# Performance work log

Hardware: AMD Instinct MI355X
Metric: run time of the kernel (lower is better)

The kernel has to match this reference:

```python
import jax, jax.numpy as jnp
import numpy as np

B, D, L, T, K = 16, 256, 256, 1000, 3
DW, DC = 4, 2  # dim_w, dim_c
CH = 8         # ConvSwishBlock out channels (10 = 1 start + 1 end + 8)


def swish(x):
    return x * jax.nn.sigmoid(x)


def setup_inputs() -> dict:
    key = jax.random.key(0)
    ks = jax.random.split(key, 12)
    # durations ~ U[1,6] per phone -> sum ~ 3.5*L ~ 896 <= T
    durations = 1.0 + 5.0 * jax.random.uniform(ks[0], (B, L), dtype=jnp.float32)
    phoneme = jax.random.normal(ks[1], (B, D, L), dtype=jnp.float32)
    # True = padded phone position
    phone_len = L - (jnp.arange(B) % 4) * 16
    phoneme_mask = (jnp.arange(L)[None, :] >= phone_len[:, None])[:, None, :]
    durations = jnp.where(phoneme_mask[:, 0, :], 0.0, durations)
    s = 0.02
    p = {
        'proj_w_W': s * jax.random.normal(ks[2], (D, D)), 'proj_w_b': jnp.zeros((D,)),
        'conv_w_W': s * jax.random.normal(ks[3], (CH, D, K)), 'conv_w_b': jnp.zeros((CH,)),
        'mlp_w_W': s * jax.random.normal(ks[4], (2 + CH, DW)), 'mlp_w_b': jnp.zeros((DW,)),
        'lin_w_W': s * jax.random.normal(ks[5], (D * DW, D)), 'lin_w_b': jnp.zeros((D,)),
        'proj_c_W': s * jax.random.normal(ks[6], (D, D)), 'proj_c_b': jnp.zeros((D,)),
        'conv_c_W': s * jax.random.normal(ks[7], (CH, D, K)), 'conv_c_b': jnp.zeros((CH,)),
        'mlp_c_W': s * jax.random.normal(ks[8], (2 + CH, DC)), 'mlp_c_b': jnp.zeros((DC,)),
        'lin_c_W': s * jax.random.normal(ks[9], (DW * DC, D)), 'lin_c_b': jnp.zeros((D,)),
    }
    return {'durations': durations, 'phoneme': phoneme, 'phoneme_mask': phoneme_mask, **p}


def _conv_branch(x, phone_pad, projW, projb, convW, convb):
    # x: (B, D, L). 1x1 conv projection, then K-wide 'same' conv to CH channels, swish, mask.
    x = jnp.einsum('od,bdl->bol', projW, x) + projb[None, :, None]
    h = jax.lax.conv_general_dilated(x, convW, (1,), 'SAME',
                                     dimension_numbers=('NCH', 'OIH', 'NCH'))
    h = swish(h + convb[None, :, None])
    h = jnp.where(phone_pad[:, None, :], 0.0, h)
    return h.transpose(0, 2, 1)  # (B, L, CH)


def _forward(durations, phoneme, phoneme_mask,
             proj_w_W, proj_w_b, conv_w_W, conv_w_b, mlp_w_W, mlp_w_b, lin_w_W, lin_w_b,
             proj_c_W, proj_c_b, conv_c_W, conv_c_b, mlp_c_W, mlp_c_b, lin_c_W, lin_c_b):
    phone_pad = phoneme_mask[:, 0, :]                       # (B, L) True = pad
    frame_len = jnp.clip(jnp.round(jnp.sum(durations, -1)), 0, T).astype(jnp.int32)
    frame_pad = jnp.arange(T)[None, :] >= frame_len[:, None]  # (B, T) True = pad
    attn_pad = frame_pad[:, :, None] | phone_pad[:, None, :]  # (B, T, L)

    sd = jnp.cumsum(durations, -1)                          # (B, L) cumulative end times
    sk = sd - durations                                     # (B, L) start times
    t = jnp.arange(1, T + 1, dtype=durations.dtype)
    S = jnp.where(attn_pad, 0.0, t[None, :, None] - sk[:, None, :])                    # (B,T,L)
    E = jnp.where(attn_pad, 0.0, jnp.broadcast_to(sd[:, None, :], attn_pad.shape)
                  - sk[:, None, :])                                                    # (B,T,L)

    # W branch: per-(frame, phone) attention weights over phones
    h_w = _conv_branch(phoneme, phone_pad, proj_w_W, proj_w_b, conv_w_W, conv_w_b)     # (B,L,CH)
    feat_w = jnp.concatenate(
        [S[..., None], E[..., None], jnp.broadcast_to(h_w[:, None], (B, T, L, CH))], -1)
    w = swish(feat_w @ mlp_w_W + mlp_w_b)                   # (B, T, L, DW)
    w = jnp.where(phone_pad[:, None, :, None], -jnp.inf, w)
    w = jax.nn.softmax(w, axis=2)                           # softmax over phones
    w = jnp.where(frame_pad[:, :, None, None], 0.0, w)

    # C branch: auxiliary per-(frame, phone) context
    h_c = _conv_branch(phoneme, phone_pad, proj_c_W, proj_c_b, conv_c_W, conv_c_b)
    feat_c = jnp.concatenate(
        [S[..., None], E[..., None], jnp.broadcast_to(h_c[:, None], (B, T, L, CH))], -1)
    c = swish(feat_c @ mlp_c_W + mlp_c_b)                   # (B, T, L, DC)

    # combine: wh = einsum over phones with phoneme features, wc with c matrix
    wh = jnp.einsum('btnq,bnh->btqh', w, phoneme.transpose(0, 2, 1))  # (B,T,DW,D)
    wh = wh.reshape(B, T, DW * D) @ lin_w_W + lin_w_b                 # (B,T,D)
    wc = jnp.einsum('btnq,btnp->btqp', w, c)                          # (B,T,DW,DC)
    wc = wc.reshape(B, T, DW * DC) @ lin_c_W + lin_c_b                # (B,T,D)
    return wh + wc


def reference(durations, phoneme, phoneme_mask,
              proj_w_W, proj_w_b, conv_w_W, conv_w_b, mlp_w_W, mlp_w_b, lin_w_W, lin_w_b,
              proj_c_W, proj_c_b, conv_c_W, conv_c_b, mlp_c_W, mlp_c_b, lin_c_W, lin_c_b):
    return _forward(durations, phoneme, phoneme_mask,
                    proj_w_W, proj_w_b, conv_w_W, conv_w_b, mlp_w_W, mlp_w_b, lin_w_W, lin_w_b,
                    proj_c_W, proj_c_b, conv_c_W, conv_c_b, mlp_c_W, mlp_c_b, lin_c_W, lin_c_b)
```

## Files before the change

kernel.cpp:

```cpp
#include <hip/hip_runtime.h>


typedef short v8s __attribute__((ext_vector_type(8)));
typedef _Float16 v8h __attribute__((ext_vector_type(8)));
typedef float f4 __attribute__((ext_vector_type(4)));

__device__ __forceinline__ float bf2f(unsigned short h) {
  return __uint_as_float(((unsigned int)h) << 16);
}
__device__ __forceinline__ unsigned short f2bf(float f) {
  unsigned int u = __float_as_uint(f);
  u = (u + 0x7FFFu + ((u >> 16) & 1u)) >> 16;
  return (unsigned short)u;
}
__device__ __forceinline__ float swishf(float x) {
  return x * __builtin_amdgcn_rcpf(1.f + __expf(-x));
}

__global__ __launch_bounds__(256) void k_prep(
    const float* __restrict__ dur, const float* __restrict__ ph,
    const float* __restrict__ liWw,
    const float* __restrict__ cvWw, const float* __restrict__ pjWw,
    const float* __restrict__ pjbw,
    const float* __restrict__ cvWc, const float* __restrict__ pjWc,
    const float* __restrict__ pjbc,
    float* __restrict__ sk, int* __restrict__ frame_len,
    unsigned short* __restrict__ Mb, float* __restrict__ bK,
    unsigned short* __restrict__ LWT, unsigned short* __restrict__ phT) {
  __shared__ float sm[32 * 33];
  int blk = blockIdx.x, tid = threadIdx.x;
  if (blk < 16) {
    int b = blk, l = tid;
    float d = dur[b * 256 + l];
    sm[l] = d;
    __syncthreads();
    for (int off = 1; off < 256; off <<= 1) {
      float v = (l >= off) ? sm[l - off] : 0.f;
      __syncthreads();
      sm[l] += v;
      __syncthreads();
    }
    sk[b * 256 + l] = sm[l] - d;
    if (l == 255) {
      int fl = (int)rintf(sm[255]);
      frame_len[b] = min(max(fl, 0), 1000);
    }
  } else if (blk < 64) {
    int x = blk - 16;
    int br = x / 24, ck = x % 24;
    int ch = ck / 3, k = ck % 3;
    const float* convW = br ? cvWc : cvWw;
    const float* projW = br ? pjWc : pjWw;
    const float* projb = br ? pjbc : pjbw;
    int d = tid;
    float acc = 0.f;
    for (int o = 0; o < 256; o++)
      acc += convW[ch * 768 + o * 3 + k] * projW[o * 256 + d];
    Mb[(br * 24 + ck) * 256 + d] = f2bf(acc);
    if (d == 0) {
      float bb = 0.f;
      for (int o = 0; o < 256; o++)
        bb += convW[ch * 768 + o * 3 + k] * projb[o];
      bK[br * 24 + ck] = bb;
    }
  } else if (blk < 320) {
    int idx = blk - 64;
    int kt = idx & 31, ot = idx >> 5;
    int tx = tid & 31, ty = tid >> 5;
#pragma unroll
    for (int r = 0; r < 4; r++) {
      int row = ty + r * 8;
      sm[row * 33 + tx] = liWw[(size_t)(kt * 32 + row) * 256 + ot * 32 + tx];
    }
    __syncthreads();
#pragma unroll
    for (int r = 0; r < 4; r++) {
      int row = ty + r * 8;
      LWT[(size_t)(ot * 32 + row) * 1024 + kt * 32 + tx] =
          f2bf(sm[tx * 33 + row]);
    }
  } else {
    int idx = blk - 320;
    int ht = idx & 7, lt = (idx >> 3) & 7, b = idx >> 6;
    int tx = tid & 31, ty = tid >> 5;
#pragma unroll
    for (int r = 0; r < 4; r++) {
      int row = ty + r * 8;
      sm[row * 33 + tx] =
          ph[(size_t)b * 65536 + (size_t)(ht * 32 + row) * 256 + lt * 32 + tx];
    }
    __syncthreads();
#pragma unroll
    for (int r = 0; r < 4; r++) {
      int row = ty + r * 8;
      phT[(size_t)b * 65536 + (size_t)(lt * 32 + row) * 256 + ht * 32 + tx] =
          f2bf(sm[tx * 33 + row]);
    }
  }
}

__global__ __launch_bounds__(256) void k_convG(
    const unsigned short* __restrict__ phT, const unsigned short* __restrict__ Mb,
    const float* __restrict__ bK, const float* __restrict__ cvbw,
    const float* __restrict__ cvbc, const float* __restrict__ dur,
    const unsigned short* __restrict__ LWT,
    float* __restrict__ hw, float* __restrict__ hc,
    _Float16* __restrict__ G) {
  __shared__ __align__(16) float C[256 * 49];
  int blk = blockIdx.x;
  int tid = threadIdx.x, wave = tid >> 6, lane = tid & 63;
  int quad = lane >> 4, col = lane & 15;
  if (blk < 16) {
    int b = blk;
    int l0 = wave * 64;
    const unsigned short* Ab = phT + (size_t)b * 65536;
    f4 acc[4][3] = {};
#pragma unroll
    for (int k0 = 0; k0 < 256; k0 += 32) {
      v8s af[4], bf[3];
#pragma unroll
      for (int lt = 0; lt < 4; lt++)
        af[lt] = *(const v8s*)(Ab + (size_t)(l0 + lt * 16 + col) * 256 + k0 + quad * 8);
#pragma unroll
      for (int ct = 0; ct < 3; ct++)
        bf[ct] = *(const v8s*)(Mb + (size_t)(ct * 16 + col) * 256 + k0 + quad * 8);
#pragma unroll
      for (int lt = 0; lt < 4; lt++)
#pragma unroll
        for (int ct = 0; ct < 3; ct++)
          acc[lt][ct] = __builtin_amdgcn_mfma_f32_16x16x32_bf16(af[lt], bf[ct],
                                                                acc[lt][ct], 0, 0, 0);
    }
#pragma unroll
    for (int lt = 0; lt < 4; lt++)
#pragma unroll
      for (int ct = 0; ct < 3; ct++)
#pragma unroll
        for (int r = 0; r < 4; r++)
          C[(l0 + lt * 16 + quad * 4 + r) * 49 + ct * 16 + col] = acc[lt][ct][r];
    __syncthreads();
    int l = tid;
    float dv = dur[b * 256 + l];
    bool vld = (dv != 0.f);
#pragma unroll
    for (int br = 0; br < 2; br++) {
      const float* convb = br ? cvbc : cvbw;
      float* dst = br ? hc : hw;
#pragma unroll
      for (int ch = 0; ch < 8; ch++) {
        int ck = br * 24 + ch * 3;
        float v = convb[ch] + bK[ck + 1] + C[l * 49 + ck + 1];
        if (l > 0) v += bK[ck + 0] + C[(l - 1) * 49 + ck + 0];
        if (l < 255) v += bK[ck + 2] + C[(l + 1) * 49 + ck + 2];
        v = swishf(v);
        dst[((size_t)(b * 256 + l)) * 8 + ch] = vld ? v : 0.f;
      }
    }
  } else {
    int idx = blk - 16;
    int b = idx >> 4;
    int sub = idx & 15;
    int q = sub >> 2, quadr = sub & 3;
    int mo = (quadr >> 1) * 128, nl = (quadr & 1) * 128;
    int wm = (wave & 1) * 64, wn = (wave >> 1) * 64;
    const unsigned short* Ag = LWT + (size_t)q * 256;
    const unsigned short* Bg = phT + (size_t)b * 65536;
    f4 acc[4][4] = {};
#pragma unroll
    for (int k0 = 0; k0 < 256; k0 += 32) {
      v8s af[4], bf[4];
#pragma unroll
      for (int mt = 0; mt < 4; mt++)
        af[mt] = *(const v8s*)(Ag + (size_t)(mo + wm + mt * 16 + col) * 1024 +
                               k0 + quad * 8);
#pragma unroll
      for (int nt = 0; nt < 4; nt++)
        bf[nt] = *(const v8s*)(Bg + (size_t)(nl + wn + nt * 16 + col) * 256 +
                               k0 + quad * 8);
#pragma unroll
      for (int mt = 0; mt < 4; mt++)
#pragma unroll
        for (int nt = 0; nt < 4; nt++)
          acc[mt][nt] = __builtin_amdgcn_mfma_f32_16x16x32_bf16(af[mt], bf[nt],
                                                                acc[mt][nt], 0, 0, 0);
    }
    _Float16* Gb = G + (size_t)b * 262144 + q * 256;
#pragma unroll
    for (int mt = 0; mt < 4; mt++)
#pragma unroll
      for (int r = 0; r < 4; r++) {
        int orow = mo + wm + mt * 16 + quad * 4 + r;
#pragma unroll
        for (int nt = 0; nt < 4; nt++) {
          int lcol = nl + wn + nt * 16 + col;
          Gb[(size_t)orow * 1024 + lcol] = (_Float16)acc[mt][nt][r];
        }
      }
  }
}

__global__ __launch_bounds__(256, 4) void k_fuse(
    const _Float16* __restrict__ G,
    const float* __restrict__ dur, const float* __restrict__ sk,
    const int* __restrict__ frame_len,
    const float* __restrict__ hw, const float* __restrict__ hc,
    const float* __restrict__ mlpWw, const float* __restrict__ mlpbw,
    const float* __restrict__ mlpWc, const float* __restrict__ mlpbc,
    const float* __restrict__ lwb, const float* __restrict__ lcb,
    const float* __restrict__ LC, float* __restrict__ out) {
  __shared__ __align__(16) _Float16 Et[2][16][264];
  __shared__ __align__(16) float4 Lbw4[256];
  __shared__ __align__(16) float4 Laux4[256];
  __shared__ float4 wredM[4];
  __shared__ float invL[16 * 4];
  __shared__ float wcL[16 * 8];

  int blk = blockIdx.x;
  int b = (blk & 7) * 2 + ((blk >> 3) & 1);
  int tile = blk >> 4;
  int t0 = tile * 16;
  int tid = threadIdx.x, wave = tid >> 6, lane = tid & 63;
  int quad = lane >> 4, col = lane & 15;

  {
    int l = tid;
    float4 a0 = *(const float4*)&hw[((size_t)(b * 256 + l)) * 8];
    float4 a1 = *(const float4*)&hw[((size_t)(b * 256 + l)) * 8 + 4];
    float4 c0 = *(const float4*)&hc[((size_t)(b * 256 + l)) * 8];
    float4 c1 = *(const float4*)&hc[((size_t)(b * 256 + l)) * 8 + 4];
    float hwv[8] = {a0.x, a0.y, a0.z, a0.w, a1.x, a1.y, a1.z, a1.w};
    float hcv[8] = {c0.x, c0.y, c0.z, c0.w, c1.x, c1.y, c1.z, c1.w};
    float dl = dur[b * 256 + l];
    float skl = sk[b * 256 + l];
    float msk = (dl != 0.f) ? 1.f : 0.f;
    float A[4];
#pragma unroll
    for (int q = 0; q < 4; q++) {
      float a = mlpbw[q] + dl * mlpWw[4 + q] - skl * mlpWw[q];
#pragma unroll
      for (int ch = 0; ch < 8; ch++) a += hwv[ch] * mlpWw[(2 + ch) * 4 + q];
      A[q] = (msk != 0.f) ? a : -1e30f;
    }
    float bb0 = mlpbc[0] + dl * mlpWc[2] - skl * mlpWc[0];
    float bb1 = mlpbc[1] + dl * mlpWc[3] - skl * mlpWc[1];
#pragma unroll
    for (int ch = 0; ch < 8; ch++) {
      bb0 += hcv[ch] * mlpWc[(2 + ch) * 2 + 0];
      bb1 += hcv[ch] * mlpWc[(2 + ch) * 2 + 1];
    }
    float4 Av = {A[0], A[1], A[2], A[3]};
    Lbw4[l] = Av;
    float4 xv = {bb0, bb1, msk, 0.f};
    Laux4[l] = xv;
    float m0 = A[0], m1 = A[1], m2 = A[2], m3 = A[3];
#pragma unroll
    for (int off = 1; off < 64; off <<= 1) {
      m0 = fmaxf(m0, __shfl_xor(m0, off));
      m1 = fmaxf(m1, __shfl_xor(m1, off));
      m2 = fmaxf(m2, __shfl_xor(m2, off));
      m3 = fmaxf(m3, __shfl_xor(m3, off));
    }
    if (lane == 0) {
      float4 mv = {m0, m1, m2, m3};
      wredM[wave] = mv;
    }
  }
  __syncthreads();
  float4 W0 = wredM[0], W1 = wredM[1], W2 = wredM[2], W3 = wredM[3];
  float maxA[4] = {fmaxf(fmaxf(W0.x, W1.x), fmaxf(W2.x, W3.x)),
                   fmaxf(fmaxf(W0.y, W1.y), fmaxf(W2.y, W3.y)),
                   fmaxf(fmaxf(W0.z, W1.z), fmaxf(W2.z, W3.z)),
                   fmaxf(fmaxf(W0.w, W1.w), fmaxf(W2.w, W3.w))};

  int fl = frame_len[b];
  int tg = tid >> 5, seg = tid & 31;
  float mw0[4] = {mlpWw[0], mlpWw[1], mlpWw[2], mlpWw[3]};
  float mc0 = mlpWc[0], mc1 = mlpWc[1];
  float tp1v[2], tS0[2], tS1[2];
  bool livev[2];
#pragma unroll
  for (int ti = 0; ti < 2; ti++) {
    int t = t0 + tg + 8 * ti;
    livev[ti] = (t < fl);
    tp1v[ti] = (float)(t + 1);
    tS0[ti] = tp1v[ti] * mc0;
    tS1[ti] = tp1v[ti] * mc1;
  }

  int wn = wave * 64;
  f4 accF[4] = {};
  const _Float16* Gb = G + (size_t)b * 262144;

#pragma unroll
  for (int pp = 0; pp < 2; pp++) {
    if (pp) __syncthreads();
    int qa = pp * 2;
    float mm[2][2];
#pragma unroll
    for (int ti = 0; ti < 2; ti++) {
      mm[ti][0] = livev[ti] ? fmaxf(maxA[qa] + tp1v[ti] * mw0[qa], 0.f) : 1e30f;
      mm[ti][1] = livev[ti] ? fmaxf(maxA[qa + 1] + tp1v[ti] * mw0[qa + 1], 0.f) : 1e30f;
    }
    float s[2][2] = {}, pw0[2][2] = {}, pw1[2][2] = {};
    for (int jj = 0; jj < 8; jj++) {
      int l = jj * 32 + seg;
      float4 A4 = Lbw4[l];
      float4 ax = Laux4[l];
      float Aa = pp ? A4.z : A4.x;
      float Ab = pp ? A4.w : A4.y;
#pragma unroll
      for (int ti = 0; ti < 2; ti++) {
        float tp1 = tp1v[ti];
        float za = Aa + tp1 * mw0[qa];
        float zb = Ab + tp1 * mw0[qa + 1];
        float ea = __expf(swishf(za) - mm[ti][0]) * ax.z;
        float eb = __expf(swishf(zb) - mm[ti][1]) * ax.z;
        float cp0 = swishf(ax.x + tS0[ti]);
        float cp1 = swishf(ax.y + tS1[ti]);
        s[ti][0] += ea;  pw0[ti][0] += ea * cp0;  pw1[ti][0] += ea * cp1;
        s[ti][1] += eb;  pw0[ti][1] += eb * cp0;  pw1[ti][1] += eb * cp1;
        Et[0][tg + 8 * ti][l] = (_Float16)ea;
        Et[1][tg + 8 * ti][l] = (_Float16)eb;
      }
    }
#pragma unroll
    for (int off = 1; off < 32; off <<= 1) {
#pragma unroll
      for (int ti = 0; ti < 2; ti++)
#pragma unroll
        for (int e2 = 0; e2 < 2; e2++) {
          s[ti][e2] += __shfl_xor(s[ti][e2], off);
          pw0[ti][e2] += __shfl_xor(pw0[ti][e2], off);
          pw1[ti][e2] += __shfl_xor(pw1[ti][e2], off);
        }
    }
    if (seg == 0) {
#pragma unroll
      for (int ti = 0; ti < 2; ti++) {
        int row = tg + 8 * ti;
#pragma unroll
        for (int e2 = 0; e2 < 2; e2++) {
          int qq = qa + e2;
          float iv = livev[ti] ? __builtin_amdgcn_rcpf(s[ti][e2]) : 0.f;
          invL[row * 4 + qq] = iv;
          wcL[row * 8 + qq * 2 + 0] = pw0[ti][e2] * iv;
          wcL[row * 8 + qq * 2 + 1] = pw1[ti][e2] * iv;
        }
      }
    }
    __syncthreads();
#pragma unroll
    for (int e2 = 0; e2 < 2; e2++) {
      int qq = qa + e2;
      f4 accq[4] = {};
#pragma unroll
      for (int k0 = 0; k0 < 256; k0 += 32) {
        v8h af = *(const v8h*)&Et[e2][col][k0 + quad * 8];
        v8h bf[4];
#pragma unroll
        for (int nt = 0; nt < 4; nt++)
          bf[nt] = *(const v8h*)(Gb + (size_t)(wn + nt * 16 + col) * 1024 +
                                 qq * 256 + k0 + quad * 8);
#pragma unroll
        for (int nt = 0; nt < 4; nt++)
          accq[nt] = __builtin_amdgcn_mfma_f32_16x16x32_f16(af, bf[nt],
                                                            accq[nt], 0, 0, 0);
      }
#pragma unroll
      for (int r = 0; r < 4; r++) {
        float iv = invL[(quad * 4 + r) * 4 + qq];
#pragma unroll
        for (int nt = 0; nt < 4; nt++) accF[nt][r] += accq[nt][r] * iv;
      }
    }
  }

#pragma unroll
  for (int nt = 0; nt < 4; nt++) {
    int oc = wn + nt * 16 + col;
    float bias = lwb[oc] + lcb[oc];
    float lc8[8];
#pragma unroll
    for (int jj = 0; jj < 8; jj++) lc8[jj] = LC[jj * 256 + oc];
#pragma unroll
    for (int r = 0; r < 4; r++) {
      int lr = quad * 4 + r;
      int trow = t0 + lr;
      if (trow < 1000) {
        float v = accF[nt][r] + bias;
#pragma unroll
        for (int jj = 0; jj < 8; jj++) v = fmaf(wcL[lr * 8 + jj], lc8[jj], v);
        out[((size_t)(b * 1000 + trow)) * 256 + oc] = v;
      }
    }
  }
}

extern "C" void kernel_launch(void* const* d_in, const int* in_sizes, int n_in,
                              void* d_out, int out_size, void* d_ws, size_t ws_size,
                              hipStream_t stream) {
  const float* dur  = (const float*)d_in[0];
  const float* ph   = (const float*)d_in[1];
  const float* pjWw = (const float*)d_in[3];
  const float* pjbw = (const float*)d_in[4];
  const float* cvWw = (const float*)d_in[5];
  const float* cvbw = (const float*)d_in[6];
  const float* mlWw = (const float*)d_in[7];
  const float* mlbw = (const float*)d_in[8];
  const float* liWw = (const float*)d_in[9];
  const float* libw = (const float*)d_in[10];
  const float* pjWc = (const float*)d_in[11];
  const float* pjbc = (const float*)d_in[12];
  const float* cvWc = (const float*)d_in[13];
  const float* cvbc = (const float*)d_in[14];
  const float* mlWc = (const float*)d_in[15];
  const float* mlbc = (const float*)d_in[16];
  const float* liWc = (const float*)d_in[17];
  const float* libc = (const float*)d_in[18];
  float* out = (float*)d_out;

  float* f = (float*)d_ws;
  size_t o = 0;
  float* sk = f + o;            o += 4096;
  int* fl = (int*)(f + o);      o += 16;
  float* bK = f + o;            o += 64;
  unsigned short* Mb = (unsigned short*)(f + o); o += 6144;
  float* hw = f + o;            o += 16 * 256 * 8;
  float* hc = f + o;            o += 16 * 256 * 8;
  _Float16* G = (_Float16*)(f + o);              o += 2097152;
  unsigned short* phT = (unsigned short*)(f + o); o += 524288;
  unsigned short* LWT = (unsigned short*)(f + o); o += 131072;

  k_prep<<<1344, 256, 0, stream>>>(dur, ph, liWw, cvWw, pjWw, pjbw, cvWc, pjWc,
                                   pjbc, sk, fl, Mb, bK, LWT, phT);
  k_convG<<<272, 256, 0, stream>>>(phT, Mb, bK, cvbw, cvbc, dur, LWT, hw, hc, G);
  k_fuse<<<1008, 256, 0, stream>>>(G, dur, sk, fl, hw, hc, mlWw, mlbw, mlWc,
                                   mlbc, libw, libc, liWc, out);
}
```

Measured before the change: 205.3 us.

## Split fused softmax-GEMM into separate softmax and tiled GEMM kernels

Breaks the fused kernel into two. k_soft computes the normalized fp16 attention weights w (B×1024×1024) and the small wc terms, writing both to workspace. k_out then runs a shared-memory-tiled MFMA GEMM of w against G, using 64×128 output tiles and register prefetch, and applies bias and the LC epilogue. This gives the GEMM proper operand reuse through LDS, whereas before each wave streamed G directly from global memory per 16-row tile. The cost is a roughly 32MB fp16 intermediate round-trip through memory and an extra launch.

```diff
diff --git a/kernel.cpp b/kernel.cpp
--- a/kernel.cpp
+++ b/kernel.cpp
@@ -199,28 +199,19 @@
   }
 }
 
-__global__ __launch_bounds__(256, 4) void k_fuse(
-    const _Float16* __restrict__ G,
+__global__ __launch_bounds__(256) void k_soft(
     const float* __restrict__ dur, const float* __restrict__ sk,
     const int* __restrict__ frame_len,
     const float* __restrict__ hw, const float* __restrict__ hc,
     const float* __restrict__ mlpWw, const float* __restrict__ mlpbw,
     const float* __restrict__ mlpWc, const float* __restrict__ mlpbc,
-    const float* __restrict__ lwb, const float* __restrict__ lcb,
-    const float* __restrict__ LC, float* __restrict__ out) {
-  __shared__ __align__(16) _Float16 Et[2][16][264];
+    _Float16* __restrict__ w, float* __restrict__ wc) {
   __shared__ __align__(16) float4 Lbw4[256];
   __shared__ __align__(16) float4 Laux4[256];
   __shared__ float4 wredM[4];
-  __shared__ float invL[16 * 4];
-  __shared__ float wcL[16 * 8];
-
-  int blk = blockIdx.x;
-  int b = (blk & 7) * 2 + ((blk >> 3) & 1);
-  int tile = blk >> 4;
-  int t0 = tile * 16;
+  int b = blockIdx.y;
+  int t0 = blockIdx.x * 16;
   int tid = threadIdx.x, wave = tid >> 6, lane = tid & 63;
-  int quad = lane >> 4, col = lane & 15;
 
   {
     int l = tid;
@@ -273,127 +264,152 @@
                    fmaxf(fmaxf(W0.w, W1.w), fmaxf(W2.w, W3.w))};
 
   int fl = frame_len[b];
-  int tg = tid >> 5, seg = tid & 31;
+  int tl = wave * 4 + (lane >> 4);
+  int l16 = lane & 15;
+  int t = t0 + tl;
+  bool live = (t < fl);
+  float tp1 = (float)(t + 1);
   float mw0[4] = {mlpWw[0], mlpWw[1], mlpWw[2], mlpWw[3]};
   float mc0 = mlpWc[0], mc1 = mlpWc[1];
-  float tp1v[2], tS0[2], tS1[2];
-  bool livev[2];
-#pragma unroll
-  for (int ti = 0; ti < 2; ti++) {
-    int t = t0 + tg + 8 * ti;
-    livev[ti] = (t < fl);
-    tp1v[ti] = (float)(t + 1);
-    tS0[ti] = tp1v[ti] * mc0;
-    tS1[ti] = tp1v[ti] * mc1;
-  }
-
-  int wn = wave * 64;
-  f4 accF[4] = {};
-  const _Float16* Gb = G + (size_t)b * 262144;
-
-#pragma unroll
-  for (int pp = 0; pp < 2; pp++) {
-    if (pp) __syncthreads();
-    int qa = pp * 2;
-    float mm[2][2];
-#pragma unroll
-    for (int ti = 0; ti < 2; ti++) {
-      mm[ti][0] = livev[ti] ? fmaxf(maxA[qa] + tp1v[ti] * mw0[qa], 0.f) : 1e30f;
-      mm[ti][1] = livev[ti] ? fmaxf(maxA[qa + 1] + tp1v[ti] * mw0[qa + 1], 0.f) : 1e30f;
-    }
-    float s[2][2] = {}, pw0[2][2] = {}, pw1[2][2] = {};
-    for (int jj = 0; jj < 8; jj++) {
-      int l = jj * 32 + seg;
-      float4 A4 = Lbw4[l];
-      float4 ax = Laux4[l];
-      float Aa = pp ? A4.z : A4.x;
-      float Ab = pp ? A4.w : A4.y;
-#pragma unroll
-      for (int ti = 0; ti < 2; ti++) {
-        float tp1 = tp1v[ti];
-        float za = Aa + tp1 * mw0[qa];
-        float zb = Ab + tp1 * mw0[qa + 1];
-        float ea = __expf(swishf(za) - mm[ti][0]) * ax.z;
-        float eb = __expf(swishf(zb) - mm[ti][1]) * ax.z;
-        float cp0 = swishf(ax.x + tS0[ti]);
-        float cp1 = swishf(ax.y + tS1[ti]);
-        s[ti][0] += ea;  pw0[ti][0] += ea * cp0;  pw1[ti][0] += ea * cp1;
-        s[ti][1] += eb;  pw0[ti][1] += eb * cp0;  pw1[ti][1] += eb * cp1;
-        Et[0][tg + 8 * ti][l] = (_Float16)ea;
-        Et[1][tg + 8 * ti][l] = (_Float16)eb;
-      }
-    }
-#pragma unroll
-    for (int off = 1; off < 32; off <<= 1) {
-#pragma unroll
-      for (int ti = 0; ti < 2; ti++)
-#pragma unroll
-        for (int e2 = 0; e2 < 2; e2++) {
-          s[ti][e2] += __shfl_xor(s[ti][e2], off);
-          pw0[ti][e2] += __shfl_xor(pw0[ti][e2], off);
-          pw1[ti][e2] += __shfl_xor(pw1[ti][e2], off);
-        }
-    }
-    if (seg == 0) {
-#pragma unroll
-      for (int ti = 0; ti < 2; ti++) {
-        int row = tg + 8 * ti;
-#pragma unroll
-        for (int e2 = 0; e2 < 2; e2++) {
-          int qq = qa + e2;
-          float iv = livev[ti] ? __builtin_amdgcn_rcpf(s[ti][e2]) : 0.f;
-          invL[row * 4 + qq] = iv;
-          wcL[row * 8 + qq * 2 + 0] = pw0[ti][e2] * iv;
-          wcL[row * 8 + qq * 2 + 1] = pw1[ti][e2] * iv;
+  float m[4];
+#pragma unroll
+  for (int q = 0; q < 4; q++)
+    m[q] = live ? fmaxf(maxA[q] + tp1 * mw0[q], 0.f) : 1e30f;
+
+  float s[4] = {}, pw[4][2] = {{}, {}, {}, {}};
+  v8h eh[4][2];
+#pragma unroll
+  for (int j = 0; j < 16; j++) {
+    int l = l16 * 16 + j;
+    float4 A4 = Lbw4[l];
+    float4 ax = Laux4[l];
+    float cp0 = swishf(ax.x + tp1 * mc0);
+    float cp1 = swishf(ax.y + tp1 * mc1);
+    float Aq[4] = {A4.x, A4.y, A4.z, A4.w};
+#pragma unroll
+    for (int q = 0; q < 4; q++) {
+      float z = Aq[q] + tp1 * mw0[q];
+      float e = __expf(swishf(z) - m[q]) * ax.z;
+      eh[q][j >> 3][j & 7] = (_Float16)e;
+      s[q] += e;
+      pw[q][0] += e * cp0;
+      pw[q][1] += e * cp1;
+    }
+  }
+#pragma unroll
+  for (int off = 1; off < 16; off <<= 1) {
+#pragma unroll
+    for (int q = 0; q < 4; q++) {
+      s[q] += __shfl_xor(s[q], off);
+      pw[q][0] += __shfl_xor(pw[q][0], off);
+      pw[q][1] += __shfl_xor(pw[q][1], off);
+    }
+  }
+  size_t base = ((size_t)b * 1024 + t) * 1024;
+#pragma unroll
+  for (int q = 0; q < 4; q++) {
+    float iv = live ? __builtin_amdgcn_rcpf(s[q]) : 0.f;
+    _Float16 ivh = (_Float16)iv;
+    v8h w0 = eh[q][0] * ivh;
+    v8h w1 = eh[q][1] * ivh;
+    *(v8h*)(w + base + q * 256 + l16 * 16) = w0;
+    *(v8h*)(w + base + q * 256 + l16 * 16 + 8) = w1;
+    if (l16 == 0 && t < 1000) {
+      wc[((size_t)(b * 1000 + t)) * 8 + q * 2 + 0] = pw[q][0] * iv;
+      wc[((size_t)(b * 1000 + t)) * 8 + q * 2 + 1] = pw[q][1] * iv;
+    }
+  }
+}
+
+__global__ __launch_bounds__(256) void k_out(const _Float16* __restrict__ w,
+                                             const _Float16* __restrict__ G,
+                                             const float* __restrict__ lwb,
+                                             const float* __restrict__ lcb,
+                                             const float* __restrict__ LC,
+                                             const float* __restrict__ wc,
+                                             float* __restrict__ out) {
+  int b = blockIdx.y;
+  int t0 = (blockIdx.x >> 1) * 64;
+  int o0 = (blockIdx.x & 1) * 128;
+  int tid = threadIdx.x, wave = tid >> 6, lane = tid & 63;
+  int quad = lane >> 4, col = lane & 15;
+  __shared__ __align__(16) _Float16 Asm[64 * 40];
+  __shared__ __align__(16) _Float16 Bsm[128 * 40];
+  __shared__ float bias_s[128];
+  __shared__ float lcs[8][128];
+  __shared__ float wcs[64][8];
+
+  for (int i = tid; i < 128; i += 256) bias_s[i] = lwb[o0 + i] + lcb[o0 + i];
+  for (int i = tid; i < 1024; i += 256)
+    lcs[i >> 7][i & 127] = LC[(i >> 7) * 256 + o0 + (i & 127)];
+  for (int i = tid; i < 512; i += 256) {
+    int r = i >> 3, j = i & 7;
+    int t = t0 + r;
+    wcs[r][j] = (t < 1000) ? wc[((size_t)(b * 1000 + t)) * 8 + j] : 0.f;
+  }
+
+  int arow = wave * 16 + (lane >> 2);
+  int aseg = lane & 3;
+  const _Float16* Ag =
+      w + (size_t)b * 1048576 + (size_t)(t0 + arow) * 1024 + aseg * 8;
+  _Float16* Al = Asm + arow * 40 + aseg * 8;
+  int brow = wave * 32 + (lane >> 2);
+  const _Float16* Bg0 =
+      G + (size_t)b * 262144 + (size_t)(o0 + brow) * 1024 + aseg * 8;
+  const _Float16* Bg1 = Bg0 + 16 * 1024;
+  _Float16* Bl0 = Bsm + brow * 40 + aseg * 8;
+  _Float16* Bl1 = Bl0 + 16 * 40;
+
+  int wm = (wave & 1) * 32, wn = (wave >> 1) * 64;
+  f4 acc[2][4] = {};
+  uint4 ra = *(const uint4*)Ag;
+  uint4 rb0 = *(const uint4*)Bg0;
+  uint4 rb1 = *(const uint4*)Bg1;
+  for (int k0 = 0; k0 < 1024; k0 += 32) {
+    __syncthreads();
+    *(uint4*)Al = ra;
+    *(uint4*)Bl0 = rb0;
+    *(uint4*)Bl1 = rb1;
+    __syncthreads();
+    if (k0 + 32 < 1024) {
+      ra = *(const uint4*)(Ag + k0 + 32);
+      rb0 = *(const uint4*)(Bg0 + k0 + 32);
+      rb1 = *(const uint4*)(Bg1 + k0 + 32);
+    }
+    v8h af[2], bf[4];
+#pragma unroll
+    for (int mt = 0; mt < 2; mt++)
+      af[mt] = *(const v8h*)(Asm + (wm + mt * 16 + col) * 40 + quad * 8);
+#pragma unroll
+    for (int nt = 0; nt < 4; nt++)
+      bf[nt] = *(const v8h*)(Bsm + (wn + nt * 16 + col) * 40 + quad * 8);
+#pragma unroll
+    for (int mt = 0; mt < 2; mt++)
+#pragma unroll
+      for (int nt = 0; nt < 4; nt++)
+        acc[mt][nt] = __builtin_amdgcn_mfma_f32_16x16x32_f16(af[mt], bf[nt],
+                                                             acc[mt][nt], 0, 0, 0);
+  }
+#pragma unroll
+  for (int mt = 0; mt < 2; mt++)
+#pragma unroll
+    for (int r = 0; r < 4; r++) {
+      int lrow = wm + mt * 16 + quad * 4 + r;
+      int trow = t0 + lrow;
+      if (trow < 1000) {
+        float4 wa = *(const float4*)&wcs[lrow][0];
+        float4 wb = *(const float4*)&wcs[lrow][4];
+        float wcl[8] = {wa.x, wa.y, wa.z, wa.w, wb.x, wb.y, wb.z, wb.w};
+#pragma unroll
+        for (int nt = 0; nt < 4; nt++) {
+          int oc = wn + nt * 16 + col;
+          float v = acc[mt][nt][r] + bias_s[oc];
+#pragma unroll
+          for (int jj = 0; jj < 8; jj++) v = fmaf(wcl[jj], lcs[jj][oc], v);
+          out[((size_t)(b * 1000 + trow)) * 256 + o0 + oc] = v;
         }
       }
     }
-    __syncthreads();
-#pragma unroll
-    for (int e2 = 0; e2 < 2; e2++) {
-      int qq = qa + e2;
-      f4 accq[4] = {};
-#pragma unroll
-      for (int k0 = 0; k0 < 256; k0 += 32) {
-        v8h af = *(const v8h*)&Et[e2][col][k0 + quad * 8];
-        v8h bf[4];
-#pragma unroll
-        for (int nt = 0; nt < 4; nt++)
-          bf[nt] = *(const v8h*)(Gb + (size_t)(wn + nt * 16 + col) * 1024 +
-                                 qq * 256 + k0 + quad * 8);
-#pragma unroll
-        for (int nt = 0; nt < 4; nt++)
-          accq[nt] = __builtin_amdgcn_mfma_f32_16x16x32_f16(af, bf[nt],
-                                                            accq[nt], 0, 0, 0);
-      }
-#pragma unroll
-      for (int r = 0; r < 4; r++) {
-        float iv = invL[(quad * 4 + r) * 4 + qq];
-#pragma unroll
-        for (int nt = 0; nt < 4; nt++) accF[nt][r] += accq[nt][r] * iv;
-      }
-    }
-  }
-
-#pragma unroll
-  for (int nt = 0; nt < 4; nt++) {
-    int oc = wn + nt * 16 + col;
-    float bias = lwb[oc] + lcb[oc];
-    float lc8[8];
-#pragma unroll
-    for (int jj = 0; jj < 8; jj++) lc8[jj] = LC[jj * 256 + oc];
-#pragma unroll
-    for (int r = 0; r < 4; r++) {
-      int lr = quad * 4 + r;
-      int trow = t0 + lr;
-      if (trow < 1000) {
-        float v = accF[nt][r] + bias;
-#pragma unroll
-        for (int jj = 0; jj < 8; jj++) v = fmaf(wcL[lr * 8 + jj], lc8[jj], v);
-        out[((size_t)(b * 1000 + trow)) * 256 + oc] = v;
-      }
-    }
-  }
 }
 
 extern "C" void kernel_launch(void* const* d_in, const int* in_sizes, int n_in,
@@ -427,13 +443,16 @@
   unsigned short* Mb = (unsigned short*)(f + o); o += 6144;
   float* hw = f + o;            o += 16 * 256 * 8;
   float* hc = f + o;            o += 16 * 256 * 8;
+  float* wc = f + o;            o += 16 * 1000 * 8;
   _Float16* G = (_Float16*)(f + o);              o += 2097152;
+  _Float16* w = (_Float16*)(f + o);              o += 8388608;
   unsigned short* phT = (unsigned short*)(f + o); o += 524288;
   unsigned short* LWT = (unsigned short*)(f + o); o += 131072;
 
   k_prep<<<1344, 256, 0, stream>>>(dur, ph, liWw, cvWw, pjWw, pjbw, cvWc, pjWc,
                                    pjbc, sk, fl, Mb, bK, LWT, phT);
   k_convG<<<272, 256, 0, stream>>>(phT, Mb, bK, cvbw, cvbc, dur, LWT, hw, hc, G);
-  k_fuse<<<1008, 256, 0, stream>>>(G, dur, sk, fl, hw, hc, mlWw, mlbw, mlWc,
-                                   mlbc, libw, libc, liWc, out);
-}
+  k_soft<<<dim3(63, 16), 256, 0, stream>>>(dur, sk, fl, hw, hc, mlWw, mlbw,
+                                           mlWc, mlbc, w, wc);
+  k_out<<<dim3(32, 16), 256, 0, stream>>>(w, G, libw, libc, liWc, wc, out);
+}
```

Result: faster. 178.2 us (-13.2%).
